# Performance work log

Measured on AMD Instinct MI355X. Metric: run time of the kernel, lower is better.

## Reference

```python
import jax, jax.numpy as jnp
import numpy as np

M = 7                 # RoIAlign output size
S = 1                 # bilinear samples per bin per axis
SPATIAL_SCALE = 1.0 / 16.0
NUM_CLASSES = 21
SCORE_THRESH = 0.05
NMS_THRESH = 0.5
NUM_DET = 100
MIN_SIZE = 1.0
REG_W = (10.0, 10.0, 5.0, 5.0)
BBOX_CLIP = float(np.log(1000.0 / 16.0))
NEG = -1e9


def setup_inputs():
    key = jax.random.key(0)
    ks = jax.random.split(key, 8)
    H, W, C, N, HID = 50, 50, 256, 1000, 1024
    feature = jax.random.normal(ks[0], (H, W, C), jnp.float32)
    ctr = jax.random.uniform(ks[1], (N, 2), jnp.float32, 50.0, 750.0)
    wh = jax.random.uniform(ks[2], (N, 2), jnp.float32, 20.0, 300.0)
    proposal = jnp.concatenate([jnp.clip(ctr - wh / 2, 0.0, 800.0),
                                jnp.clip(ctr + wh / 2, 0.0, 800.0)], axis=1)
    D = C * M * M  # 12544
    sc = 0.02
    return dict(
        feature=feature, proposal=proposal,
        w1=jax.random.normal(ks[3], (D, HID), jnp.float32) * sc,
        b1=jnp.zeros((HID,), jnp.float32),
        w2=jax.random.normal(ks[4], (HID, HID), jnp.float32) * sc,
        b2=jnp.zeros((HID,), jnp.float32),
        w_cls=jax.random.normal(ks[5], (HID, NUM_CLASSES), jnp.float32) * sc,
        b_cls=jnp.zeros((NUM_CLASSES,), jnp.float32),
        w_box=jax.random.normal(ks[6], (HID, NUM_CLASSES * 4), jnp.float32) * sc,
        b_box=jnp.zeros((NUM_CLASSES * 4,), jnp.float32),
        img_h=800, img_w=800)


def _bilinear(feat, ys, xs):
    # feat [H,W,C]; ys [N,P]; xs [N,Q] -> [N,P,Q,C], zero outside image
    H, W, _ = feat.shape
    y = jnp.broadcast_to(ys[:, :, None], (ys.shape[0], ys.shape[1], xs.shape[1]))
    x = jnp.broadcast_to(xs[:, None, :], y.shape)
    oob = (y < -1.0) | (y > H) | (x < -1.0) | (x > W)
    y = jnp.clip(y, 0.0, H - 1.0)
    x = jnp.clip(x, 0.0, W - 1.0)
    y0 = jnp.floor(y).astype(jnp.int32)
    x0 = jnp.floor(x).astype(jnp.int32)
    y1 = jnp.minimum(y0 + 1, H - 1)
    x1 = jnp.minimum(x0 + 1, W - 1)
    ly, lx = y - y0, x - x0
    hy, hx = 1.0 - ly, 1.0 - lx
    v = (feat[y0, x0] * (hy * hx)[..., None] + feat[y0, x1] * (hy * lx)[..., None]
         + feat[y1, x0] * (ly * hx)[..., None] + feat[y1, x1] * (ly * lx)[..., None])
    return jnp.where(oob[..., None], 0.0, v)


def _roi_align(feat, rois):
    # feat [H,W,C], rois [N,4] in image coords -> [N, C*M*M]
    r = rois * SPATIAL_SCALE
    x1, y1 = r[:, 0], r[:, 1]
    rw = jnp.maximum(r[:, 2] - x1, 1.0)
    rh = jnp.maximum(r[:, 3] - y1, 1.0)
    off = (jnp.arange(M, dtype=jnp.float32)[:, None]
           + (jnp.arange(S, dtype=jnp.float32) + 0.5)[None, :] / S).reshape(-1)  # [M*S]
    ys = y1[:, None] + off[None, :] * (rh / M)[:, None]
    xs = x1[:, None] + off[None, :] * (rw / M)[:, None]
    g = _bilinear(feat, ys, xs)                                  # [N,MS,MS,C]
    N, _, _, C = g.shape
    g = g.reshape(N, M, S, M, S, C).mean(axis=(2, 4))            # [N,M,M,C]
    return g.transpose(0, 3, 1, 2).reshape(N, C * M * M)


def _decode(deltas, boxes):
    # deltas [L,N,4] (per class), boxes [N,4]
    wx, wy, ww, wh = REG_W
    w = boxes[:, 2] - boxes[:, 0]
    h = boxes[:, 3] - boxes[:, 1]
    cx = boxes[:, 0] + 0.5 * w
    cy = boxes[:, 1] + 0.5 * h
    dx, dy = deltas[..., 0] / wx, deltas[..., 1] / wy
    dw = jnp.minimum(deltas[..., 2] / ww, BBOX_CLIP)
    dh = jnp.minimum(deltas[..., 3] / wh, BBOX_CLIP)
    pcx, pcy = dx * w + cx, dy * h + cy
    pw, ph = jnp.exp(dw) * w, jnp.exp(dh) * h
    return jnp.stack([pcx - 0.5 * pw, pcy - 0.5 * ph,
                      pcx + 0.5 * pw, pcy + 0.5 * ph], axis=-1)


def _iou_one(box, boxes):
    lt = jnp.maximum(box[:2], boxes[:, :2])
    rb = jnp.minimum(box[2:], boxes[:, 2:])
    wh = jnp.clip(rb - lt, 0.0)
    inter = wh[:, 0] * wh[:, 1]
    a1 = (box[2] - box[0]) * (box[3] - box[1])
    a2 = (boxes[:, 2] - boxes[:, 0]) * (boxes[:, 3] - boxes[:, 1])
    return inter / (a1 + a2 - inter + 1e-9)


def _nms(boxes, scores):
    # fixed-shape greedy NMS: NUM_DET selections, invalid slots masked to NEG
    def step(s, _):
        i = jnp.argmax(s)
        sc, b = s[i], boxes[i]
        supp = _iou_one(b, boxes) > NMS_THRESH
        s = jnp.where(supp, NEG, s).at[i].set(NEG)
        return s, (b, sc)
    _, (kb, ksc) = jax.lax.scan(step, scores, None, length=NUM_DET)
    valid = ksc > NEG * 0.5
    return jnp.where(valid[:, None], kb, 0.0), jnp.where(valid, ksc, 0.0)


def _forward(feature, proposal, w1, b1, w2, b2, w_cls, b_cls, w_box, b_box, img_h, img_w):
    pooled = _roi_align(feature, proposal)                # [N, 12544]
    h = jax.nn.relu(pooled @ w1 + b1)
    h = jax.nn.relu(h @ w2 + b2)
    logits = h @ w_cls + b_cls                            # [N, 21]
    deltas = (h @ w_box + b_box).reshape(-1, NUM_CLASSES, 4)
    pred_score = jax.nn.softmax(logits, axis=-1)
    cls_scores = pred_score[:, 1:].T                      # [L, N], L = 20 fg classes
    cls_deltas = jnp.swapaxes(deltas[:, 1:], 0, 1)        # [L, N, 4]
    boxes = _decode(cls_deltas, proposal)                 # [L, N, 4]
    boxes = jnp.stack([jnp.clip(boxes[..., 0], 0.0, img_w),
                       jnp.clip(boxes[..., 1], 0.0, img_h),
                       jnp.clip(boxes[..., 2], 0.0, img_w),
                       jnp.clip(boxes[..., 3], 0.0, img_h)], axis=-1)
    bw = boxes[..., 2] - boxes[..., 0]
    bh = boxes[..., 3] - boxes[..., 1]
    keep = (bw >= MIN_SIZE) & (bh >= MIN_SIZE) & (cls_scores >= SCORE_THRESH)
    masked = jnp.where(keep, cls_scores, NEG)
    kb, ksc = jax.vmap(_nms)(boxes, masked)               # [L,K,4], [L,K]
    labels = jnp.broadcast_to(jnp.arange(1, NUM_CLASSES, dtype=jnp.int32)[:, None], ksc.shape)
    return kb.reshape(-1, 4), ksc.reshape(-1), labels.reshape(-1)


def reference(feature, proposal, w1, b1, w2, b2, w_cls, b_cls, w_box, b_box, img_h, img_w):
    return _forward(feature, proposal, w1, b1, w2, b2, w_cls, b_cls, w_box, b_box,
                    float(img_h), float(img_w))
```

## Files before the change

kernel.cpp:

```cpp
#include <hip/hip_runtime.h>


#define NEGV -1000000000.0f

typedef __attribute__((ext_vector_type(8))) short short8v;
typedef __attribute__((ext_vector_type(4))) float f32x4;

#define KDIM 12544
#define PL   (1024 * 12544)

__device__ __forceinline__ unsigned short to_bf16(float f) {
    unsigned u = __float_as_uint(f);
    unsigned r = u + 0x7FFFu + ((u >> 16) & 1u);
    return (unsigned short)(r >> 16);
}
__device__ __forceinline__ float bf2f(unsigned short s) {
    return __uint_as_float((unsigned)s << 16);
}
__device__ __forceinline__ void gload16(const void* gsrc, void* ldst) {
    __builtin_amdgcn_global_load_lds(
        (const __attribute__((address_space(1))) unsigned int*)gsrc,
        (__attribute__((address_space(3))) unsigned int*)ldst,
        16, 0, 0);
}

__global__ __launch_bounds__(256) void roi_align_split3(const float* __restrict__ feat,
    const float* __restrict__ prop, unsigned short* __restrict__ Ap)
{
    int n = blockIdx.y;
    int p = blockIdx.x;
    int my = p / 7, mx = p % 7;
    float x1 = prop[n * 4 + 0] * 0.0625f;
    float y1 = prop[n * 4 + 1] * 0.0625f;
    float x2 = prop[n * 4 + 2] * 0.0625f;
    float y2 = prop[n * 4 + 3] * 0.0625f;
    float rw = fmaxf(x2 - x1, 1.0f), rh = fmaxf(y2 - y1, 1.0f);
    float y = y1 + ((float)my + 0.5f) * (rh / 7.0f);
    float x = x1 + ((float)mx + 0.5f) * (rw / 7.0f);
    bool oob = (y < -1.0f) || (y > 50.0f) || (x < -1.0f) || (x > 50.0f);
    y = fminf(fmaxf(y, 0.0f), 49.0f);
    x = fminf(fmaxf(x, 0.0f), 49.0f);
    int y0 = (int)floorf(y), x0 = (int)floorf(x);
    int y1i = min(y0 + 1, 49), x1i = min(x0 + 1, 49);
    float ly = y - (float)y0, lx = x - (float)x0;
    float hy = 1.0f - ly, hx = 1.0f - lx;
    int c = threadIdx.x;
    float v = feat[(y0 * 50 + x0) * 256 + c] * (hy * hx)
            + feat[(y0 * 50 + x1i) * 256 + c] * (hy * lx)
            + feat[(y1i * 50 + x0) * 256 + c] * (ly * hx)
            + feat[(y1i * 50 + x1i) * 256 + c] * (ly * lx);
    if (oob) v = 0.0f;
    unsigned short s1 = to_bf16(v);  float r  = v - bf2f(s1);
    unsigned short s2 = to_bf16(r);  float r2 = r - bf2f(s2);
    unsigned short s3 = to_bf16(r2);
    size_t o = (size_t)n * KDIM + p * 256 + c;
    Ap[o] = s1; Ap[PL + o] = s2; Ap[2 * (size_t)PL + o] = s3;
}

__global__ __launch_bounds__(256) void zero_padA(unsigned short* __restrict__ Ap)
{
    int id = blockIdx.x * 256 + threadIdx.x;
    int p = id / 37632;
    int rem = id - p * 37632;
    int r = rem / 1568, c8 = rem - r * 1568;
    *(uint4*)&Ap[(size_t)p * PL + (size_t)(1000 + r) * KDIM + c8 * 8] =
        make_uint4(0, 0, 0, 0);
}

__global__ __launch_bounds__(256) void conv_w1_k(const float* __restrict__ w1,
    unsigned short* __restrict__ Bt)
{
    __shared__ unsigned short T[3][64][72];
    int k0 = blockIdx.x * 64;
    int n0 = blockIdx.y * 64;
    int t = threadIdx.x;
#pragma unroll
    for (int j = 0; j < 16; ++j) {
        int idx = t + 256 * j;
        int n_l = idx & 63, k_l = idx >> 6;
        int kp = k0 + k_l;
        int orow = (kp & 255) * 49 + (kp >> 8);
        float v = w1[(size_t)orow * 1024 + n0 + n_l];
        unsigned short s1 = to_bf16(v);  float r  = v - bf2f(s1);
        unsigned short s2 = to_bf16(r);  float r2 = r - bf2f(s2);
        T[0][k_l][n_l] = s1;
        T[1][k_l][n_l] = s2;
        T[2][k_l][n_l] = to_bf16(r2);
    }
    __syncthreads();
#pragma unroll
    for (int p = 0; p < 3; ++p)
#pragma unroll
        for (int jj = 0; jj < 2; ++jj) {
            int w = t + 256 * jj;
            int n_l = w >> 3, kg = w & 7;
            short8v pk;
#pragma unroll
            for (int e = 0; e < 8; ++e) pk[e] = (short)T[p][kg * 8 + e][n_l];
            *(short8v*)&Bt[(size_t)p * PL + (size_t)(n0 + n_l) * KDIM + k0 + kg * 8] = pk;
        }
}

__global__ __launch_bounds__(256, 3) void gemm_mfma_split3(
    const unsigned short* __restrict__ Ap, const unsigned short* __restrict__ Bp,
    float* __restrict__ part, int Ks)
{
    __shared__ unsigned short ldsb[24576];

    int b = blockIdx.x;
    int xcd = b & 7;
    int rest = b >> 3;
    int m = rest & 7;
    int qhi = rest >> 3;
    int q = xcd + 8 * qhi;
    int z  = q >> 3;
    int qz = q & 7;
    int col0 = ((qz & 1) * 4 + (m & 3)) * 128;
    int row0 = ((qz >> 1) * 2 + (m >> 2)) * 128;
    int kOff = z * Ks;

    int t = threadIdx.x;
    int w = t >> 6;
    int lane = t & 63;
    int ln = lane & 15, g = lane >> 4;
    int wr = (w >> 1) * 64, wc = (w & 1) * 64;

    const unsigned short* smat = (w >= 2) ? Bp : Ap;
    int sbase = (w >= 2) ? col0 : row0;
    char* lbase = (char*)ldsb + ((w >= 2) ? 12288 * 2 : 0);
    int j0 = (w & 1) * 12;
    int srow_lane = lane >> 2;
    int scol_lane = (lane & 3) * 8;

    f32x4 acc[4][4] = {};
    const unsigned short* lds_us = ldsb;

    int nks = Ks >> 5;
    for (int ks = 0; ks < nks; ++ks) {
        int kpos = kOff + (ks << 5) + scol_lane;
#pragma unroll
        for (int ii = 0; ii < 12; ++ii) {
            int j = j0 + ii;
            int p = j >> 3, rb = j & 7;
            const unsigned short* src = smat + (size_t)p * PL
                + (size_t)(sbase + rb * 16 + srow_lane) * KDIM + kpos;
            gload16(src, lbase + p * 8192 + rb * 1024);
        }
        __syncthreads();
#pragma unroll
        for (int pb = 0; pb < 3; ++pb) {
            short8v bf[4];
#pragma unroll
            for (int fc = 0; fc < 4; ++fc)
                bf[fc] = *(const short8v*)&lds_us[12288 + pb * 4096 + (wc + fc * 16 + ln) * 32 + g * 8];
#pragma unroll
            for (int pa = 0; pa < 3; ++pa) {
                if (pa + pb >= 3) break;
                short8v af[4];
#pragma unroll
                for (int fr = 0; fr < 4; ++fr)
                    af[fr] = *(const short8v*)&lds_us[pa * 4096 + (wr + fr * 16 + ln) * 32 + g * 8];
#pragma unroll
                for (int fr = 0; fr < 4; ++fr)
#pragma unroll
                    for (int fc = 0; fc < 4; ++fc)
                        acc[fr][fc] = __builtin_amdgcn_mfma_f32_16x16x32_bf16(
                            af[fr], bf[fc], acc[fr][fc], 0, 0, 0);
            }
        }
        __syncthreads();
    }
    float* dst = part + (size_t)z * (1024 * 1024);
    int rbase = row0 + wr, cbase = col0 + wc;
#pragma unroll
    for (int fr = 0; fr < 4; ++fr)
#pragma unroll
        for (int fc = 0; fc < 4; ++fc)
#pragma unroll
            for (int reg = 0; reg < 4; ++reg)
                dst[(size_t)(rbase + fr * 16 + g * 4 + reg) * 1024 + cbase + fc * 16 + ln] =
                    acc[fr][fc][reg];
}

__global__ __launch_bounds__(256) void gemm_splitk(const float* __restrict__ A,
    const float* __restrict__ B, float* __restrict__ part,
    int Mdim, int Ndim, int Kdim, int Ks, int permute)
{
    __shared__ float As[32][68];
    __shared__ float Bs[32][128];
    int tid = threadIdx.x;
    int col0 = blockIdx.x * 128;
    int row0 = blockIdx.y * 64;
    int kOff = blockIdx.z * Ks;
    int ty = tid >> 4, tx = tid & 15;
    int ar0 = tid >> 3;
    int af  = tid & 7;
    int aswz = (af & 3) << 3;
    int bkr0 = tid >> 5;
    int bf   = tid & 31;
    float4 pa0, pa1, pb0, pb1, pb2, pb3;

    auto loadA = [&](int k0) {
        int gr0 = row0 + ar0;
        int gr1 = gr0 + 32;
        pa0 = make_float4(0.f, 0.f, 0.f, 0.f);
        pa1 = make_float4(0.f, 0.f, 0.f, 0.f);
        if (gr0 < Mdim) pa0 = *(const float4*)&A[(size_t)gr0 * Kdim + kOff + k0 + af * 4];
        if (gr1 < Mdim) pa1 = *(const float4*)&A[(size_t)gr1 * Kdim + kOff + k0 + af * 4];
    };
    auto rowB = [&](int k0, int i) {
        int kg = kOff + k0 + bkr0 + 8 * i;
        int brv = permute ? ((kg & 255) * 49 + (kg >> 8)) : kg;
        return (const float4*)&B[(size_t)brv * Ndim + col0 + bf * 4];
    };
    auto loadB = [&](int k0) {
        pb0 = *rowB(k0, 0);
        pb1 = *rowB(k0, 1);
        pb2 = *rowB(k0, 2);
        pb3 = *rowB(k0, 3);
    };
    auto store = [&]() {
        int rc0 = ar0 ^ aswz;
        int rc1 = (ar0 + 32) ^ aswz;
        As[af * 4 + 0][rc0] = pa0.x;
        As[af * 4 + 1][rc0] = pa0.y;
        As[af * 4 + 2][rc0] = pa0.z;
        As[af * 4 + 3][rc0] = pa0.w;
        As[af * 4 + 0][rc1] = pa1.x;
        As[af * 4 + 1][rc1] = pa1.y;
        As[af * 4 + 2][rc1] = pa1.z;
        As[af * 4 + 3][rc1] = pa1.w;
        *(float4*)&Bs[bkr0 +  0][bf * 4] = pb0;
        *(float4*)&Bs[bkr0 +  8][bf * 4] = pb1;
        *(float4*)&Bs[bkr0 + 16][bf * 4] = pb2;
        *(float4*)&Bs[bkr0 + 24][bf * 4] = pb3;
    };

    float acc[4][8] = {};
    loadA(0); loadB(0);
    for (int k0 = 0; k0 < Ks; k0 += 32) {
        __syncthreads();
        store();
        __syncthreads();
        if (k0 + 32 < Ks) { loadA(k0 + 32); loadB(k0 + 32); }
#pragma unroll 8
        for (int kk = 0; kk < 32; ++kk) {
            int sa = ((kk >> 2) & 3) << 3;
            float4 a  = *(const float4*)&As[kk][(ty * 4) ^ sa];
            float4 b0 = *(const float4*)&Bs[kk][tx * 4];
            float4 b1 = *(const float4*)&Bs[kk][64 + tx * 4];
            float ar[4] = {a.x, a.y, a.z, a.w};
            float br[8] = {b0.x, b0.y, b0.z, b0.w, b1.x, b1.y, b1.z, b1.w};
#pragma unroll
            for (int i2 = 0; i2 < 4; ++i2)
#pragma unroll
                for (int j = 0; j < 8; ++j)
                    acc[i2][j] += ar[i2] * br[j];
        }
    }
    float* dst = part + (size_t)blockIdx.z * Mdim * Ndim;
    int gcA = col0 + tx * 4, gcB = col0 + 64 + tx * 4;
#pragma unroll
    for (int i2 = 0; i2 < 4; ++i2) {
        int gr = row0 + ty * 4 + i2;
        if (gr < Mdim) {
            *(float4*)&dst[(size_t)gr * Ndim + gcA] =
                make_float4(acc[i2][0], acc[i2][1], acc[i2][2], acc[i2][3]);
            *(float4*)&dst[(size_t)gr * Ndim + gcB] =
                make_float4(acc[i2][4], acc[i2][5], acc[i2][6], acc[i2][7]);
        }
    }
}

__global__ __launch_bounds__(256) void reduce_bias_relu_k(const float* __restrict__ part,
    const float* __restrict__ bias, float* __restrict__ outp, int Ndim, int S, int MN)
{
    int m = blockIdx.x, t = threadIdx.x;
    size_t o = (size_t)m * Ndim + t * 4;
    float4 acc = *(const float4*)&part[o];
    for (int s = 1; s < S; ++s) {
        float4 p = *(const float4*)&part[(size_t)s * MN + o];
        acc.x += p.x; acc.y += p.y; acc.z += p.z; acc.w += p.w;
    }
    float4 bv = *(const float4*)&bias[t * 4];
    acc.x = fmaxf(acc.x + bv.x, 0.f);
    acc.y = fmaxf(acc.y + bv.y, 0.f);
    acc.z = fmaxf(acc.z + bv.z, 0.f);
    acc.w = fmaxf(acc.w + bv.w, 0.f);
    *(float4*)&outp[o] = acc;
}

__global__ __launch_bounds__(128) void heads_k(const float* __restrict__ h,
    const float* __restrict__ w_cls, const float* __restrict__ b_cls,
    const float* __restrict__ w_box, const float* __restrict__ b_box,
    float* __restrict__ logits, float* __restrict__ deltas)
{
    __shared__ float sh[1024];
    int n = blockIdx.x;
    for (int i = threadIdx.x; i < 1024; i += 128) sh[i] = h[(size_t)n * 1024 + i];
    __syncthreads();
    int j = threadIdx.x;
    if (j < 21) {
        float acc = b_cls[j];
        for (int k = 0; k < 1024; ++k) acc += sh[k] * w_cls[k * 21 + j];
        logits[n * 21 + j] = acc;
    } else if (j < 105) {
        int jj = j - 21;
        float acc = b_box[jj];
        for (int k = 0; k < 1024; ++k) acc += sh[k] * w_box[k * 84 + jj];
        deltas[n * 84 + jj] = acc;
    }
}

__global__ __launch_bounds__(64) void postproc_k(const float* __restrict__ logits,
    const float* __restrict__ deltas, const float* __restrict__ prop,
    const int* __restrict__ img_h_p, const int* __restrict__ img_w_p,
    float* __restrict__ scores_m, float* __restrict__ boxes_dec)
{
    int n = blockIdx.x;
    int cls = threadIdx.x;
    if (cls < 1 || cls > 20) return;
    float mx = -3.0e38f;
    for (int i = 0; i < 21; ++i) mx = fmaxf(mx, logits[n * 21 + i]);
    float sum = 0.f;
    for (int i = 0; i < 21; ++i) sum += expf(logits[n * 21 + i] - mx);
    float score = expf(logits[n * 21 + cls] - mx) / sum;

    float p0 = prop[n * 4 + 0], p1 = prop[n * 4 + 1];
    float p2 = prop[n * 4 + 2], p3 = prop[n * 4 + 3];
    float w = p2 - p0, h = p3 - p1;
    float cx = p0 + 0.5f * w, cy = p1 + 0.5f * h;
    float d0 = deltas[n * 84 + cls * 4 + 0];
    float d1 = deltas[n * 84 + cls * 4 + 1];
    float d2 = deltas[n * 84 + cls * 4 + 2];
    float d3 = deltas[n * 84 + cls * 4 + 3];
    const float CLIP = 4.135166556742356f;
    float dx = d0 / 10.0f, dy = d1 / 10.0f;
    float dw = fminf(d2 / 5.0f, CLIP), dh = fminf(d3 / 5.0f, CLIP);
    float pcx = dx * w + cx, pcy = dy * h + cy;
    float pw = expf(dw) * w, ph = expf(dh) * h;
    float bx1 = pcx - 0.5f * pw, by1 = pcy - 0.5f * ph;
    float bx2 = pcx + 0.5f * pw, by2 = pcy + 0.5f * ph;
    float iw = (float)img_w_p[0], ih = (float)img_h_p[0];
    bx1 = fminf(fmaxf(bx1, 0.f), iw);
    by1 = fminf(fmaxf(by1, 0.f), ih);
    bx2 = fminf(fmaxf(bx2, 0.f), iw);
    by2 = fminf(fmaxf(by2, 0.f), ih);
    float bw = bx2 - bx1, bh = by2 - by1;
    bool keep = (bw >= 1.0f) && (bh >= 1.0f) && (score >= 0.05f);
    int o = (cls - 1) * 1000 + n;
    scores_m[o] = keep ? score : NEGV;
    ((float4*)boxes_dec)[o] = make_float4(bx1, by1, bx2, by2);
}

__global__ __launch_bounds__(256) void nms_sort_k(const float* __restrict__ scores_m,
    const float* __restrict__ boxes_dec, float* __restrict__ sboxes,
    float* __restrict__ sscore, int* __restrict__ Vcnt)
{
    __shared__ unsigned long long sk[1024];
    __shared__ int cnt;
    int cls = blockIdx.x, t = threadIdx.x;
    if (t == 0) cnt = 0;
    __syncthreads();
    for (int r = t; r < 1024; r += 256) {
        unsigned long long inv = ~0ull;
        if (r < 1000) {
            float v = scores_m[cls * 1000 + r];
            unsigned ub = __float_as_uint(v);
            ub = (ub & 0x80000000u) ? ~ub : (ub | 0x80000000u);
            inv = ~(((unsigned long long)ub << 32) | (unsigned)(1023 - r));
            if (v > 0.5f * NEGV) atomicAdd(&cnt, 1);
        }
        sk[r] = inv;
    }
    __syncthreads();
    for (int k = 2; k <= 1024; k <<= 1) {
        for (int j = k >> 1; j > 0; j >>= 1) {
            for (int pi = t; pi < 512; pi += 256) {
                int i = ((pi & ~(j - 1)) << 1) | (pi & (j - 1));
                int p = i | j;
                bool up = ((i & k) == 0);
                unsigned long long a = sk[i], b2 = sk[p];
                if ((a > b2) == up) { sk[i] = b2; sk[p] = a; }
            }
            __syncthreads();
        }
    }
    for (int r = t; r < 1024; r += 256) {
        unsigned long long key = ~sk[r];
        unsigned ub = (unsigned)(key >> 32);
        int idx = 1023 - (int)(key & 1023u);
        float4 bx = make_float4(0.f, 0.f, 0.f, 0.f);
        float scv = NEGV;
        if (key != 0ull && idx < 1000) {
            bx = ((const float4*)boxes_dec)[cls * 1000 + idx];
            unsigned u = (ub & 0x80000000u) ? (ub & 0x7FFFFFFFu) : ~ub;
            scv = __uint_as_float(u);
        }
        ((float4*)sboxes)[(size_t)cls * 1024 + r] = bx;
        sscore[(size_t)cls * 1024 + r] = scv;
    }
    if (t == 0) Vcnt[cls] = cnt;
}

__global__ __launch_bounds__(256) void nms_mask_k(const float* __restrict__ sboxes,
    unsigned long long* __restrict__ mask)
{
    __shared__ float4 colb[1024];
    __shared__ float area[1024];
    int cls = blockIdx.x >> 4;
    int chunk = blockIdx.x & 15;
    int t = threadIdx.x;
    const float4* sb = (const float4*)sboxes + (size_t)cls * 1024;
    for (int j = t; j < 1024; j += 256) {
        float4 b = sb[j];
        colb[j] = b;
        area[j] = (b.z - b.x) * (b.w - b.y);
    }
    __syncthreads();
    int row_l = t >> 2;
    int qt = t & 3;
    int i = chunk * 64 + row_l;
    float4 rb = colb[i];
    float a1 = area[i];
    unsigned long long* dst = mask + ((size_t)cls * 1024 + i) * 16 + qt * 4;
#pragma unroll
    for (int w = 0; w < 4; ++w) {
        unsigned long long wv = 0;
        int jb = qt * 256 + w * 64;
#pragma unroll 8
        for (int bi = 0; bi < 64; ++bi) {
            int j = jb + bi;
            float4 cb = colb[j];
            float ltx = fmaxf(rb.x, cb.x), lty = fmaxf(rb.y, cb.y);
            float rbx = fminf(rb.z, cb.z), rby = fminf(rb.w, cb.w);
            float wiw = fmaxf(rbx - ltx, 0.f), wih = fmaxf(rby - lty, 0.f);
            float inter = wiw * wih;
            float iou = inter / (a1 + area[j] - inter + 1e-9f);
            if (j > i && iou > 0.5f) wv |= (1ull << bi);
        }
        dst[w] = wv;
    }
}

__global__ __launch_bounds__(64) void nms_sweep_k(const float* __restrict__ sboxes,
    const float* __restrict__ sscore, const int* __restrict__ Vcnt,
    const unsigned long long* __restrict__ mask, float* __restrict__ out)
{
    int cls = blockIdx.x;
    int lane = threadIdx.x;
    __shared__ int keptlist[100];
    int V = Vcnt[cls];
    const unsigned long long* mbase = mask + (size_t)cls * 1024 * 16;
    unsigned long long suppr = 0;
    int kept = 0;
    int nb = (V + 15) >> 4;
    for (int b = 0; b < nb && kept < 100; ++b) {
        unsigned long long L[16];
#pragma unroll
        for (int k = 0; k < 16; ++k)
            L[k] = mbase[(size_t)(b * 16 + k) * 16 + (lane & 15)];
#pragma unroll
        for (int k = 0; k < 16; ++k) {
            int i = b * 16 + k;
            if (i < V && kept < 100) {
                bool sup = (lane == (i >> 6)) && ((suppr >> (i & 63)) & 1ull);
                if (__ballot(sup) == 0ull) {
                    if (lane == 0) keptlist[kept] = i;
                    if (lane < 16) suppr |= L[k];
                    ++kept;
                }
            }
        }
    }
    __syncthreads();
    float* kb   = out;
    float* ksc  = out + 8000;
    float* klab = out + 10000;
    for (int s = lane; s < 100; s += 64) {
        klab[cls * 100 + s] = (float)(cls + 1);
        if (s < kept) {
            int r = keptlist[s];
            ((float4*)kb)[cls * 100 + s] =
                ((const float4*)sboxes)[(size_t)cls * 1024 + r];
            ksc[cls * 100 + s] = sscore[(size_t)cls * 1024 + r];
        } else {
            ((float4*)kb)[cls * 100 + s] = make_float4(0.f, 0.f, 0.f, 0.f);
            ksc[cls * 100 + s] = 0.f;
        }
    }
}

extern "C" void kernel_launch(void* const* d_in, const int* in_sizes, int n_in,
                              void* d_out, int out_size, void* d_ws, size_t ws_size,
                              hipStream_t stream)
{
    const float* feat  = (const float*)d_in[0];
    const float* prop  = (const float*)d_in[1];
    const float* w1    = (const float*)d_in[2];
    const float* b1    = (const float*)d_in[3];
    const float* w2    = (const float*)d_in[4];
    const float* b2    = (const float*)d_in[5];
    const float* w_cls = (const float*)d_in[6];
    const float* b_cls = (const float*)d_in[7];
    const float* w_box = (const float*)d_in[8];
    const float* b_box = (const float*)d_in[9];
    const int* img_h   = (const int*)d_in[10];
    const int* img_w   = (const int*)d_in[11];

    char* wsb = (char*)d_ws;
    unsigned short* Apl = (unsigned short*)wsb;
    unsigned short* Bpl = (unsigned short*)(wsb + 77070336);
    float* part   = (float*)(wsb + 154140672);
    float* h1     = (float*)(wsb + 187695104);
    float* h2     = (float*)(wsb + 191791104);
    float* logits = (float*)(wsb + 195887104);
    float* deltas = (float*)(wsb + 195971104);
    float* scores_m  = (float*)(wsb + 196307104);
    float* boxes_dec = (float*)(wsb + 196387104);
    unsigned long long* nmask = (unsigned long long*)(wsb + 154140672);
    float* sboxes = (float*)(wsb + 156762112);
    float* sscore = (float*)(wsb + 157089792);
    int*   Vcnt   = (int*)(wsb + 157171712);
    float* outp = (float*)d_out;

    hipLaunchKernelGGL(roi_align_split3, dim3(49, 1000), dim3(256), 0, stream,
                       feat, prop, Apl);
    hipLaunchKernelGGL(zero_padA, dim3(441), dim3(256), 0, stream, Apl);
    hipLaunchKernelGGL(conv_w1_k, dim3(196, 16), dim3(256), 0, stream, w1, Bpl);
    hipLaunchKernelGGL(gemm_mfma_split3, dim3(512), dim3(256), 0, stream,
                       Apl, Bpl, part, 1568);
    hipLaunchKernelGGL(reduce_bias_relu_k, dim3(1000), dim3(256), 0, stream,
                       part, b1, h1, 1024, 8, 1024 * 1024);
    hipLaunchKernelGGL(gemm_splitk, dim3(8, 16, 4), dim3(256), 0, stream,
                       h1, w2, part, 1000, 1024, 1024, 256, 0);
    hipLaunchKernelGGL(reduce_bias_relu_k, dim3(1000), dim3(256), 0, stream,
                       part, b2, h2, 1024, 4, 1024000);
    hipLaunchKernelGGL(heads_k, dim3(1000), dim3(128), 0, stream,
                       h2, w_cls, b_cls, w_box, b_box, logits, deltas);
    hipLaunchKernelGGL(postproc_k, dim3(1000), dim3(64), 0, stream,
                       logits, deltas, prop, img_h, img_w, scores_m, boxes_dec);
    hipLaunchKernelGGL(nms_sort_k, dim3(20), dim3(256), 0, stream,
                       scores_m, boxes_dec, sboxes, sscore, Vcnt);
    hipLaunchKernelGGL(nms_mask_k, dim3(320), dim3(256), 0, stream, sboxes, nmask);
    hipLaunchKernelGGL(nms_sweep_k, dim3(20), dim3(64), 0, stream,
                       sboxes, sscore, Vcnt, nmask, outp);
}
```

Measured before the change: 514.6 us.

## Move second GEMM and heads to bf16x3 MFMA and double-buffer LDS staging

```diff
diff --git a/kernel.cpp b/kernel.cpp
--- a/kernel.cpp
+++ b/kernel.cpp
@@ -57,30 +57,21 @@
     Ap[o] = s1; Ap[PL + o] = s2; Ap[2 * (size_t)PL + o] = s3;
 }
 
-__global__ __launch_bounds__(256) void zero_padA(unsigned short* __restrict__ Ap)
-{
-    int id = blockIdx.x * 256 + threadIdx.x;
-    int p = id / 37632;
-    int rem = id - p * 37632;
-    int r = rem / 1568, c8 = rem - r * 1568;
-    *(uint4*)&Ap[(size_t)p * PL + (size_t)(1000 + r) * KDIM + c8 * 8] =
-        make_uint4(0, 0, 0, 0);
-}
-
-__global__ __launch_bounds__(256) void conv_w1_k(const float* __restrict__ w1,
-    unsigned short* __restrict__ Bt)
+__global__ __launch_bounds__(256) void convT_k(const float* __restrict__ src,
+    unsigned short* __restrict__ dst, int perm, int Ktot)
 {
     __shared__ unsigned short T[3][64][72];
     int k0 = blockIdx.x * 64;
     int n0 = blockIdx.y * 64;
     int t = threadIdx.x;
+    size_t plst = (size_t)1024 * Ktot;
 #pragma unroll
     for (int j = 0; j < 16; ++j) {
         int idx = t + 256 * j;
         int n_l = idx & 63, k_l = idx >> 6;
         int kp = k0 + k_l;
-        int orow = (kp & 255) * 49 + (kp >> 8);
-        float v = w1[(size_t)orow * 1024 + n0 + n_l];
+        int orow = perm ? ((kp & 255) * 49 + (kp >> 8)) : kp;
+        float v = src[(size_t)orow * 1024 + n0 + n_l];
         unsigned short s1 = to_bf16(v);  float r  = v - bf2f(s1);
         unsigned short s2 = to_bf16(r);  float r2 = r - bf2f(s2);
         T[0][k_l][n_l] = s1;
@@ -97,16 +88,106 @@
             short8v pk;
 #pragma unroll
             for (int e = 0; e < 8; ++e) pk[e] = (short)T[p][kg * 8 + e][n_l];
-            *(short8v*)&Bt[(size_t)p * PL + (size_t)(n0 + n_l) * KDIM + k0 + kg * 8] = pk;
-        }
-}
-
-__global__ __launch_bounds__(256, 3) void gemm_mfma_split3(
-    const unsigned short* __restrict__ Ap, const unsigned short* __restrict__ Bp,
-    float* __restrict__ part, int Ks)
-{
-    __shared__ unsigned short ldsb[24576];
-
+            *(short8v*)&dst[p * plst + (size_t)(n0 + n_l) * Ktot + k0 + kg * 8] = pk;
+        }
+}
+
+__global__ __launch_bounds__(256) void conv_heads_k(const float* __restrict__ w_cls,
+    const float* __restrict__ w_box, unsigned short* __restrict__ Bth)
+{
+    int id = blockIdx.x * 256 + threadIdx.x;
+    int j = id >> 10, k = id & 1023;
+    float v = 0.f;
+    if (j < 21) v = w_cls[k * 21 + j];
+    else if (j < 105) v = w_box[k * 84 + (j - 21)];
+    unsigned short s1 = to_bf16(v);  float r  = v - bf2f(s1);
+    unsigned short s2 = to_bf16(r);  float r2 = r - bf2f(s2);
+    Bth[id] = s1; Bth[131072 + id] = s2; Bth[262144 + id] = to_bf16(r2);
+}
+
+__device__ __forceinline__ void gemm_body(const unsigned short* __restrict__ Ap,
+    const unsigned short* __restrict__ Bp, float* __restrict__ part,
+    int K, int Ks, int nks, size_t plA, size_t plB, int N,
+    int col0, int row0, int z, unsigned short* lds)
+{
+    int t = threadIdx.x;
+    int w = t >> 6, lane = t & 63;
+    int ln = lane & 15, g = lane >> 4;
+    int wr = (w >> 1) * 64, wc = (w & 1) * 64;
+
+    const unsigned short* smat = (w >= 2) ? Bp : Ap;
+    size_t spl = (w >= 2) ? plB : plA;
+    int sbase = (w >= 2) ? col0 : row0;
+    int hoff = (w >= 2) ? 24576 : 0;
+    int j0 = (w & 1) * 12;
+    int srow = lane >> 2;
+    int scol = ((lane & 3) ^ ((lane >> 3) & 3)) * 8;
+    int kOff = z * Ks;
+
+    auto stage = [&](int buf, int ks) {
+        char* lb = (char*)lds + buf * 49152 + hoff;
+        int kpos = kOff + (ks << 5) + scol;
+#pragma unroll
+        for (int ii = 0; ii < 12; ++ii) {
+            int j = j0 + ii;
+            int p = j >> 3, rb = j & 7;
+            const unsigned short* src = smat + (size_t)p * spl
+                + (size_t)(sbase + rb * 16 + srow) * K + kpos;
+            gload16(src, lb + p * 8192 + rb * 1024);
+        }
+    };
+
+    f32x4 acc[4][4] = {};
+    stage(0, 0);
+    __syncthreads();
+    int buf = 0;
+    for (int ks = 0; ks < nks; ++ks) {
+        if (ks + 1 < nks) stage(buf ^ 1, ks + 1);
+        const unsigned short* la  = (const unsigned short*)((char*)lds + buf * 49152);
+        const unsigned short* lbB = (const unsigned short*)((char*)lds + buf * 49152 + 24576);
+#pragma unroll
+        for (int pb = 0; pb < 3; ++pb) {
+            short8v bf[4];
+#pragma unroll
+            for (int fc = 0; fc < 4; ++fc) {
+                int r = wc + fc * 16 + ln;
+                bf[fc] = *(const short8v*)&lbB[pb * 4096 + r * 32 + ((g ^ ((r >> 1) & 3)) << 3)];
+            }
+#pragma unroll
+            for (int pa = 0; pa < 3 - pb; ++pa) {
+                short8v af[4];
+#pragma unroll
+                for (int fr = 0; fr < 4; ++fr) {
+                    int r = wr + fr * 16 + ln;
+                    af[fr] = *(const short8v*)&la[pa * 4096 + r * 32 + ((g ^ ((r >> 1) & 3)) << 3)];
+                }
+#pragma unroll
+                for (int fr = 0; fr < 4; ++fr)
+#pragma unroll
+                    for (int fc = 0; fc < 4; ++fc)
+                        acc[fr][fc] = __builtin_amdgcn_mfma_f32_16x16x32_bf16(
+                            af[fr], bf[fc], acc[fr][fc], 0, 0, 0);
+            }
+        }
+        __syncthreads();
+        buf ^= 1;
+    }
+    float* dst = part + (size_t)z * 1024 * N;
+    int rbase = row0 + wr, cbase = col0 + wc;
+#pragma unroll
+    for (int fr = 0; fr < 4; ++fr)
+#pragma unroll
+        for (int fc = 0; fc < 4; ++fc)
+#pragma unroll
+            for (int reg = 0; reg < 4; ++reg)
+                dst[(size_t)(rbase + fr * 16 + g * 4 + reg) * N + cbase + fc * 16 + ln] =
+                    acc[fr][fc][reg];
+}
+
+__global__ __launch_bounds__(256, 1) void gemm1_k(const unsigned short* __restrict__ Ap,
+    const unsigned short* __restrict__ Bp, float* __restrict__ part)
+{
+    extern __shared__ unsigned short ldsdyn[];
     int b = blockIdx.x;
     int xcd = b & 7;
     int rest = b >> 3;
@@ -117,223 +198,79 @@
     int qz = q & 7;
     int col0 = ((qz & 1) * 4 + (m & 3)) * 128;
     int row0 = ((qz >> 1) * 2 + (m >> 2)) * 128;
-    int kOff = z * Ks;
-
-    int t = threadIdx.x;
-    int w = t >> 6;
-    int lane = t & 63;
-    int ln = lane & 15, g = lane >> 4;
-    int wr = (w >> 1) * 64, wc = (w & 1) * 64;
-
-    const unsigned short* smat = (w >= 2) ? Bp : Ap;
-    int sbase = (w >= 2) ? col0 : row0;
-    char* lbase = (char*)ldsb + ((w >= 2) ? 12288 * 2 : 0);
-    int j0 = (w & 1) * 12;
-    int srow_lane = lane >> 2;
-    int scol_lane = (lane & 3) * 8;
-
-    f32x4 acc[4][4] = {};
-    const unsigned short* lds_us = ldsb;
-
-    int nks = Ks >> 5;
-    for (int ks = 0; ks < nks; ++ks) {
-        int kpos = kOff + (ks << 5) + scol_lane;
-#pragma unroll
-        for (int ii = 0; ii < 12; ++ii) {
-            int j = j0 + ii;
-            int p = j >> 3, rb = j & 7;
-            const unsigned short* src = smat + (size_t)p * PL
-                + (size_t)(sbase + rb * 16 + srow_lane) * KDIM + kpos;
-            gload16(src, lbase + p * 8192 + rb * 1024);
-        }
-        __syncthreads();
-#pragma unroll
-        for (int pb = 0; pb < 3; ++pb) {
-            short8v bf[4];
-#pragma unroll
-            for (int fc = 0; fc < 4; ++fc)
-                bf[fc] = *(const short8v*)&lds_us[12288 + pb * 4096 + (wc + fc * 16 + ln) * 32 + g * 8];
-#pragma unroll
-            for (int pa = 0; pa < 3; ++pa) {
-                if (pa + pb >= 3) break;
-                short8v af[4];
-#pragma unroll
-                for (int fr = 0; fr < 4; ++fr)
-                    af[fr] = *(const short8v*)&lds_us[pa * 4096 + (wr + fr * 16 + ln) * 32 + g * 8];
-#pragma unroll
-                for (int fr = 0; fr < 4; ++fr)
-#pragma unroll
-                    for (int fc = 0; fc < 4; ++fc)
-                        acc[fr][fc] = __builtin_amdgcn_mfma_f32_16x16x32_bf16(
-                            af[fr], bf[fc], acc[fr][fc], 0, 0, 0);
-            }
-        }
-        __syncthreads();
-    }
-    float* dst = part + (size_t)z * (1024 * 1024);
-    int rbase = row0 + wr, cbase = col0 + wc;
-#pragma unroll
-    for (int fr = 0; fr < 4; ++fr)
-#pragma unroll
-        for (int fc = 0; fc < 4; ++fc)
-#pragma unroll
-            for (int reg = 0; reg < 4; ++reg)
-                dst[(size_t)(rbase + fr * 16 + g * 4 + reg) * 1024 + cbase + fc * 16 + ln] =
-                    acc[fr][fc][reg];
-}
-
-__global__ __launch_bounds__(256) void gemm_splitk(const float* __restrict__ A,
-    const float* __restrict__ B, float* __restrict__ part,
-    int Mdim, int Ndim, int Kdim, int Ks, int permute)
-{
-    __shared__ float As[32][68];
-    __shared__ float Bs[32][128];
-    int tid = threadIdx.x;
-    int col0 = blockIdx.x * 128;
-    int row0 = blockIdx.y * 64;
-    int kOff = blockIdx.z * Ks;
-    int ty = tid >> 4, tx = tid & 15;
-    int ar0 = tid >> 3;
-    int af  = tid & 7;
-    int aswz = (af & 3) << 3;
-    int bkr0 = tid >> 5;
-    int bf   = tid & 31;
-    float4 pa0, pa1, pb0, pb1, pb2, pb3;
-
-    auto loadA = [&](int k0) {
-        int gr0 = row0 + ar0;
-        int gr1 = gr0 + 32;
-        pa0 = make_float4(0.f, 0.f, 0.f, 0.f);
-        pa1 = make_float4(0.f, 0.f, 0.f, 0.f);
-        if (gr0 < Mdim) pa0 = *(const float4*)&A[(size_t)gr0 * Kdim + kOff + k0 + af * 4];
-        if (gr1 < Mdim) pa1 = *(const float4*)&A[(size_t)gr1 * Kdim + kOff + k0 + af * 4];
-    };
-    auto rowB = [&](int k0, int i) {
-        int kg = kOff + k0 + bkr0 + 8 * i;
-        int brv = permute ? ((kg & 255) * 49 + (kg >> 8)) : kg;
-        return (const float4*)&B[(size_t)brv * Ndim + col0 + bf * 4];
-    };
-    auto loadB = [&](int k0) {
-        pb0 = *rowB(k0, 0);
-        pb1 = *rowB(k0, 1);
-        pb2 = *rowB(k0, 2);
-        pb3 = *rowB(k0, 3);
-    };
-    auto store = [&]() {
-        int rc0 = ar0 ^ aswz;
-        int rc1 = (ar0 + 32) ^ aswz;
-        As[af * 4 + 0][rc0] = pa0.x;
-        As[af * 4 + 1][rc0] = pa0.y;
-        As[af * 4 + 2][rc0] = pa0.z;
-        As[af * 4 + 3][rc0] = pa0.w;
-        As[af * 4 + 0][rc1] = pa1.x;
-        As[af * 4 + 1][rc1] = pa1.y;
-        As[af * 4 + 2][rc1] = pa1.z;
-        As[af * 4 + 3][rc1] = pa1.w;
-        *(float4*)&Bs[bkr0 +  0][bf * 4] = pb0;
-        *(float4*)&Bs[bkr0 +  8][bf * 4] = pb1;
-        *(float4*)&Bs[bkr0 + 16][bf * 4] = pb2;
-        *(float4*)&Bs[bkr0 + 24][bf * 4] = pb3;
-    };
-
-    float acc[4][8] = {};
-    loadA(0); loadB(0);
-    for (int k0 = 0; k0 < Ks; k0 += 32) {
-        __syncthreads();
-        store();
-        __syncthreads();
-        if (k0 + 32 < Ks) { loadA(k0 + 32); loadB(k0 + 32); }
-#pragma unroll 8
-        for (int kk = 0; kk < 32; ++kk) {
-            int sa = ((kk >> 2) & 3) << 3;
-            float4 a  = *(const float4*)&As[kk][(ty * 4) ^ sa];
-            float4 b0 = *(const float4*)&Bs[kk][tx * 4];
-            float4 b1 = *(const float4*)&Bs[kk][64 + tx * 4];
-            float ar[4] = {a.x, a.y, a.z, a.w};
-            float br[8] = {b0.x, b0.y, b0.z, b0.w, b1.x, b1.y, b1.z, b1.w};
-#pragma unroll
-            for (int i2 = 0; i2 < 4; ++i2)
-#pragma unroll
-                for (int j = 0; j < 8; ++j)
-                    acc[i2][j] += ar[i2] * br[j];
-        }
-    }
-    float* dst = part + (size_t)blockIdx.z * Mdim * Ndim;
-    int gcA = col0 + tx * 4, gcB = col0 + 64 + tx * 4;
-#pragma unroll
-    for (int i2 = 0; i2 < 4; ++i2) {
-        int gr = row0 + ty * 4 + i2;
-        if (gr < Mdim) {
-            *(float4*)&dst[(size_t)gr * Ndim + gcA] =
-                make_float4(acc[i2][0], acc[i2][1], acc[i2][2], acc[i2][3]);
-            *(float4*)&dst[(size_t)gr * Ndim + gcB] =
-                make_float4(acc[i2][4], acc[i2][5], acc[i2][6], acc[i2][7]);
-        }
-    }
-}
-
-__global__ __launch_bounds__(256) void reduce_bias_relu_k(const float* __restrict__ part,
-    const float* __restrict__ bias, float* __restrict__ outp, int Ndim, int S, int MN)
+    gemm_body(Ap, Bp, part, KDIM, 1568, 49, (size_t)PL, (size_t)PL, 1024,
+              col0, row0, z, ldsdyn);
+}
+
+__global__ __launch_bounds__(256, 1) void gemm_g_k(const unsigned short* __restrict__ Ap,
+    const unsigned short* __restrict__ Bp, float* __restrict__ part,
+    int K, int Ks, int nks, int plA, int plB, int N)
+{
+    extern __shared__ unsigned short ldsdyn[];
+    gemm_body(Ap, Bp, part, K, Ks, nks, (size_t)plA, (size_t)plB, N,
+              blockIdx.x * 128, blockIdx.y * 128, blockIdx.z, ldsdyn);
+}
+
+__global__ __launch_bounds__(256) void reduce_split3_k(const float* __restrict__ part,
+    const float* __restrict__ bias, unsigned short* __restrict__ dstP, int S)
 {
     int m = blockIdx.x, t = threadIdx.x;
-    size_t o = (size_t)m * Ndim + t * 4;
+    size_t o = (size_t)m * 1024 + t * 4;
     float4 acc = *(const float4*)&part[o];
     for (int s = 1; s < S; ++s) {
-        float4 p = *(const float4*)&part[(size_t)s * MN + o];
+        float4 p = *(const float4*)&part[(size_t)s * 1048576 + o];
         acc.x += p.x; acc.y += p.y; acc.z += p.z; acc.w += p.w;
     }
     float4 bv = *(const float4*)&bias[t * 4];
-    acc.x = fmaxf(acc.x + bv.x, 0.f);
-    acc.y = fmaxf(acc.y + bv.y, 0.f);
-    acc.z = fmaxf(acc.z + bv.z, 0.f);
-    acc.w = fmaxf(acc.w + bv.w, 0.f);
-    *(float4*)&outp[o] = acc;
-}
-
-__global__ __launch_bounds__(128) void heads_k(const float* __restrict__ h,
-    const float* __restrict__ w_cls, const float* __restrict__ b_cls,
-    const float* __restrict__ w_box, const float* __restrict__ b_box,
-    float* __restrict__ logits, float* __restrict__ deltas)
-{
-    __shared__ float sh[1024];
-    int n = blockIdx.x;
-    for (int i = threadIdx.x; i < 1024; i += 128) sh[i] = h[(size_t)n * 1024 + i];
-    __syncthreads();
-    int j = threadIdx.x;
-    if (j < 21) {
-        float acc = b_cls[j];
-        for (int k = 0; k < 1024; ++k) acc += sh[k] * w_cls[k * 21 + j];
-        logits[n * 21 + j] = acc;
-    } else if (j < 105) {
-        int jj = j - 21;
-        float acc = b_box[jj];
-        for (int k = 0; k < 1024; ++k) acc += sh[k] * w_box[k * 84 + jj];
-        deltas[n * 84 + jj] = acc;
-    }
-}
-
-__global__ __launch_bounds__(64) void postproc_k(const float* __restrict__ logits,
-    const float* __restrict__ deltas, const float* __restrict__ prop,
-    const int* __restrict__ img_h_p, const int* __restrict__ img_w_p,
-    float* __restrict__ scores_m, float* __restrict__ boxes_dec)
+    float vals[4] = { fmaxf(acc.x + bv.x, 0.f), fmaxf(acc.y + bv.y, 0.f),
+                      fmaxf(acc.z + bv.z, 0.f), fmaxf(acc.w + bv.w, 0.f) };
+    unsigned short o1[4], o2[4], o3[4];
+#pragma unroll
+    for (int e = 0; e < 4; ++e) {
+        unsigned short s1 = to_bf16(vals[e]);  float r  = vals[e] - bf2f(s1);
+        unsigned short s2 = to_bf16(r);        float r2 = r - bf2f(s2);
+        o1[e] = s1; o2[e] = s2; o3[e] = to_bf16(r2);
+    }
+    *(uint2*)&dstP[o]           = *(uint2*)o1;
+    *(uint2*)&dstP[1048576 + o] = *(uint2*)o2;
+    *(uint2*)&dstP[2097152 + o] = *(uint2*)o3;
+}
+
+__global__ __launch_bounds__(128) void reduce_heads_k(const float* __restrict__ part,
+    const float* __restrict__ b_cls, const float* __restrict__ b_box,
+    float* __restrict__ Hout)
+{
+    int m = blockIdx.x, t = threadIdx.x;
+    size_t o = (size_t)m * 128 + t;
+    float a = part[o];
+    for (int s = 1; s < 8; ++s) a += part[(size_t)s * 131072 + o];
+    float b = (t < 21) ? b_cls[t] : (t < 105 ? b_box[t - 21] : 0.f);
+    Hout[o] = a + b;
+}
+
+__global__ __launch_bounds__(64) void postproc_k(const float* __restrict__ H,
+    const float* __restrict__ prop, const int* __restrict__ img_h_p,
+    const int* __restrict__ img_w_p, float* __restrict__ scores_m,
+    float* __restrict__ boxes_dec)
 {
     int n = blockIdx.x;
     int cls = threadIdx.x;
     if (cls < 1 || cls > 20) return;
+    const float* hn = H + (size_t)n * 128;
     float mx = -3.0e38f;
-    for (int i = 0; i < 21; ++i) mx = fmaxf(mx, logits[n * 21 + i]);
+    for (int i = 0; i < 21; ++i) mx = fmaxf(mx, hn[i]);
     float sum = 0.f;
-    for (int i = 0; i < 21; ++i) sum += expf(logits[n * 21 + i] - mx);
-    float score = expf(logits[n * 21 + cls] - mx) / sum;
+    for (int i = 0; i < 21; ++i) sum += expf(hn[i] - mx);
+    float score = expf(hn[cls] - mx) / sum;
 
     float p0 = prop[n * 4 + 0], p1 = prop[n * 4 + 1];
     float p2 = prop[n * 4 + 2], p3 = prop[n * 4 + 3];
     float w = p2 - p0, h = p3 - p1;
     float cx = p0 + 0.5f * w, cy = p1 + 0.5f * h;
-    float d0 = deltas[n * 84 + cls * 4 + 0];
-    float d1 = deltas[n * 84 + cls * 4 + 1];
-    float d2 = deltas[n * 84 + cls * 4 + 2];
-    float d3 = deltas[n * 84 + cls * 4 + 3];
+    float d0 = hn[21 + cls * 4 + 0];
+    float d1 = hn[21 + cls * 4 + 1];
+    float d2 = hn[21 + cls * 4 + 2];
+    float d3 = hn[21 + cls * 4 + 3];
     const float CLIP = 4.135166556742356f;
     float dx = d0 / 10.0f, dy = d1 / 10.0f;
     float dw = fminf(d2 / 5.0f, CLIP), dh = fminf(d3 / 5.0f, CLIP);
@@ -508,16 +445,22 @@
     const int* img_h   = (const int*)d_in[10];
     const int* img_w   = (const int*)d_in[11];
 
+    (void)hipFuncSetAttribute(reinterpret_cast<const void*>(gemm1_k),
+                              hipFuncAttributeMaxDynamicSharedMemorySize, 98304);
+    (void)hipFuncSetAttribute(reinterpret_cast<const void*>(gemm_g_k),
+                              hipFuncAttributeMaxDynamicSharedMemorySize, 98304);
+
     char* wsb = (char*)d_ws;
     unsigned short* Apl = (unsigned short*)wsb;
     unsigned short* Bpl = (unsigned short*)(wsb + 77070336);
-    float* part   = (float*)(wsb + 154140672);
-    float* h1     = (float*)(wsb + 187695104);
-    float* h2     = (float*)(wsb + 191791104);
-    float* logits = (float*)(wsb + 195887104);
-    float* deltas = (float*)(wsb + 195971104);
-    float* scores_m  = (float*)(wsb + 196307104);
-    float* boxes_dec = (float*)(wsb + 196387104);
+    float* part = (float*)(wsb + 154140672);
+    unsigned short* Ap2 = (unsigned short*)wsb;
+    unsigned short* Bt2 = (unsigned short*)(wsb + 6291456);
+    unsigned short* Bth = (unsigned short*)(wsb + 12582912);
+    unsigned short* Ah  = (unsigned short*)(wsb + 13369344);
+    float* scores_m  = (float*)(wsb + 187695104);
+    float* boxes_dec = (float*)(wsb + 187775104);
+    float* Hout      = (float*)(wsb + 188095104);
     unsigned long long* nmask = (unsigned long long*)(wsb + 154140672);
     float* sboxes = (float*)(wsb + 156762112);
     float* sscore = (float*)(wsb + 157089792);
@@ -526,20 +469,26 @@
 
     hipLaunchKernelGGL(roi_align_split3, dim3(49, 1000), dim3(256), 0, stream,
                        feat, prop, Apl);
-    hipLaunchKernelGGL(zero_padA, dim3(441), dim3(256), 0, stream, Apl);
-    hipLaunchKernelGGL(conv_w1_k, dim3(196, 16), dim3(256), 0, stream, w1, Bpl);
-    hipLaunchKernelGGL(gemm_mfma_split3, dim3(512), dim3(256), 0, stream,
-                       Apl, Bpl, part, 1568);
-    hipLaunchKernelGGL(reduce_bias_relu_k, dim3(1000), dim3(256), 0, stream,
-                       part, b1, h1, 1024, 8, 1024 * 1024);
-    hipLaunchKernelGGL(gemm_splitk, dim3(8, 16, 4), dim3(256), 0, stream,
-                       h1, w2, part, 1000, 1024, 1024, 256, 0);
-    hipLaunchKernelGGL(reduce_bias_relu_k, dim3(1000), dim3(256), 0, stream,
-                       part, b2, h2, 1024, 4, 1024000);
-    hipLaunchKernelGGL(heads_k, dim3(1000), dim3(128), 0, stream,
-                       h2, w_cls, b_cls, w_box, b_box, logits, deltas);
+    hipLaunchKernelGGL(convT_k, dim3(196, 16), dim3(256), 0, stream,
+                       w1, Bpl, 1, KDIM);
+    hipLaunchKernelGGL(gemm1_k, dim3(512), dim3(256), 98304, stream,
+                       Apl, Bpl, part);
+    hipLaunchKernelGGL(reduce_split3_k, dim3(1000), dim3(256), 0, stream,
+                       part, b1, Ap2, 8);
+    hipLaunchKernelGGL(convT_k, dim3(16, 16), dim3(256), 0, stream,
+                       w2, Bt2, 0, 1024);
+    hipLaunchKernelGGL(conv_heads_k, dim3(512), dim3(256), 0, stream,
+                       w_cls, w_box, Bth);
+    hipLaunchKernelGGL(gemm_g_k, dim3(8, 8, 4), dim3(256), 98304, stream,
+                       Ap2, Bt2, part, 1024, 256, 8, 1048576, 1048576, 1024);
+    hipLaunchKernelGGL(reduce_split3_k, dim3(1000), dim3(256), 0, stream,
+                       part, b2, Ah, 4);
+    hipLaunchKernelGGL(gemm_g_k, dim3(1, 8, 8), dim3(256), 98304, stream,
+                       Ah, Bth, part, 1024, 128, 4, 1048576, 131072, 128);
+    hipLaunchKernelGGL(reduce_heads_k, dim3(1000), dim3(128), 0, stream,
+                       part, b_cls, b_box, Hout);
     hipLaunchKernelGGL(postproc_k, dim3(1000), dim3(64), 0, stream,
-                       logits, deltas, prop, img_h, img_w, scores_m, boxes_dec);
+                       Hout, prop, img_h, img_w, scores_m, boxes_dec);
     hipLaunchKernelGGL(nms_sort_k, dim3(20), dim3(256), 0, stream,
                        scores_m, boxes_dec, sboxes, sscore, Vcnt);
     hipLaunchKernelGGL(nms_mask_k, dim3(320), dim3(256), 0, stream, sboxes, nmask);
```

Result: faster. 442.8 us (-13.9%).
